# Performance work log

Measured on AMD Instinct MI355X. Metric: run time of the kernel, lower is better.

Reference implementation:

```python
import jax, jax.numpy as jnp
import numpy as np

B, S, FEAT, HID, H = 8, 1024, 1024, 1024, 8
DH = HID // H  # head dim = 128
MASK_VAL = -128.0  # mask_val = -2**7 (soft additive mask, per original code)


def setup_inputs() -> dict:
    key = jax.random.key(0)
    ks = jax.random.split(key, 4)
    scale = 0.02
    return {
        "queries": jax.random.normal(ks[0], (B, S, FEAT), dtype=jnp.float32),
        "Wq": jax.random.normal(ks[1], (FEAT, HID), dtype=jnp.float32) * scale,
        "bq": jnp.zeros((HID,), dtype=jnp.float32),
        "Wk": jax.random.normal(ks[2], (FEAT, HID), dtype=jnp.float32) * scale,
        "bk": jnp.zeros((HID,), dtype=jnp.float32),
        "Wv": jax.random.normal(ks[3], (FEAT, HID), dtype=jnp.float32) * scale,
        "bv": jnp.zeros((HID,), dtype=jnp.float32),
    }


def reference(queries, Wq, bq, Wk, bk, Wv, bv):
    # Self-attention: keys = values = queries (torch forward defaults)
    q = queries @ Wq + bq  # [B,S,HID]
    k = queries @ Wk + bk
    v = queries @ Wv + bv
    # split heads: chunk along last dim == reshape (B,S,H,DH)
    qh = q.reshape(B, S, H, DH)
    kh = k.reshape(B, S, H, DH)
    vh = v.reshape(B, S, H, DH)
    # exp-scaled-dot score (non-standard: exp BEFORE mask/softmax)
    logits = jnp.einsum("bqhd,bkhd->bhqk", qh, kh) / np.float32(np.sqrt(DH))
    score = jnp.exp(logits)
    # soft additive causal mask: upper triangle (diag=1) gets -128
    mask = jnp.triu(jnp.full((S, S), MASK_VAL, dtype=score.dtype), k=1)
    att = jax.nn.softmax(score + mask, axis=-1)  # [B,H,S,S]
    ctx = jnp.einsum("bhqk,bkhd->bqhd", att, vh)  # [B,S,H,DH]
    # reverse heads: concat along last dim
    return ctx.reshape(B, S, HID)
```

## Files before the change

kernel.cpp:

```cpp
#include <hip/hip_runtime.h>


typedef __bf16 bf16x8 __attribute__((ext_vector_type(8)));
typedef float floatx4 __attribute__((ext_vector_type(4)));
typedef unsigned short u16;
typedef unsigned int u32;

#define RSCALE 0.08838834764831845f

__device__ __forceinline__ u16 f2b(float f) {
  union { float f; unsigned u; } v; v.f = f;
  return (u16)((v.u + 0x7FFFu + ((v.u >> 16) & 1u)) >> 16);
}

__device__ __forceinline__ void gld_lds16(const void* g, void* l) {
  __builtin_amdgcn_global_load_lds(
      (const __attribute__((address_space(1))) unsigned*)g,
      (__attribute__((address_space(3))) unsigned*)l, 16, 0, 0);
}

#define MFMA16(a, b, c) __builtin_amdgcn_mfma_f32_16x16x32_bf16(a, b, c, 0, 0, 0)

__global__ __launch_bounds__(256) void prep_kernel(
    const float4* __restrict__ X, u16* __restrict__ Xb,
    const float* __restrict__ Wq, const float* __restrict__ Wk,
    const float* __restrict__ Wv, u16* __restrict__ Wtb) {
  if (blockIdx.x < 8192) {
    unsigned i = blockIdx.x * 256u + threadIdx.x;
    float4 v = X[i];
    ushort4 o;
    o.x = f2b(v.x); o.y = f2b(v.y); o.z = f2b(v.z); o.w = f2b(v.w);
    *reinterpret_cast<ushort4*>(Xb + 4u * i) = o;
  } else {
    const int bid = blockIdx.x - 8192;
    const int mat = bid >> 10;
    const int bx = bid & 31, by = (bid >> 5) & 31;
    const float* W = (mat == 0) ? Wq : (mat == 1) ? Wk : Wv;
    u16* Wt = Wtb + (size_t)mat * (1024u * 1024u);
    __shared__ u16 tile[32][33];
    const int x = threadIdx.x & 31, y = threadIdx.x >> 5;
    const int kt = bx * 32, nt = by * 32;
#pragma unroll
    for (int i = 0; i < 4; ++i)
      tile[y + 8 * i][x] = f2b(W[(size_t)(kt + y + 8 * i) * 1024 + nt + x]);
    __syncthreads();
#pragma unroll
    for (int i = 0; i < 4; ++i)
      Wt[(size_t)(nt + y + 8 * i) * 1024 + kt + x] = tile[x][y + 8 * i];
  }
}

__global__ __launch_bounds__(256, 4) void gemm_qkv_kernel(
    const u16* __restrict__ Xb, const u16* __restrict__ Wtb,
    const float* __restrict__ bq, const float* __restrict__ bk,
    const float* __restrict__ bv, u16* __restrict__ Qh, u16* __restrict__ Kh,
    u16* __restrict__ Vt) {
  const int mat = blockIdx.z;
  const u16* __restrict__ Wt = Wtb + (size_t)mat * (1024u * 1024u);
  const float* __restrict__ bias = (mat == 0) ? bq : (mat == 1) ? bk : bv;

  const int m0 = blockIdx.x * 128;
  const int n0 = blockIdx.y * 128;

  __shared__ u16 As[2][128 * 32];
  __shared__ u16 Bs[2][128 * 32];

  const int tid = threadIdx.x;
  const int wid = tid >> 6;
  const int lane = tid & 63;
  const int quad = lane >> 4;
  const int l16 = lane & 15;
  const int wm = (wid & 1) * 64;
  const int wn = (wid >> 1) * 64;

  const floatx4 z4 = {0.f, 0.f, 0.f, 0.f};
  floatx4 acc[4][4];
#pragma unroll
  for (int i = 0; i < 4; ++i)
#pragma unroll
    for (int j = 0; j < 4; ++j) acc[i][j] = z4;

  const int srow = lane >> 2;
  const int sg = (lane & 3) ^ ((lane >> 4) & 3);

  auto stage = [&](int b, int k0) {
#pragma unroll
    for (int c = 0; c < 2; ++c) {
      const int r0 = wid * 32 + c * 16;
      gld_lds16(Xb + (size_t)(m0 + r0 + srow) * 1024 + k0 + sg * 8,
                As[b] + r0 * 32);
      gld_lds16(Wt + (size_t)(n0 + r0 + srow) * 1024 + k0 + sg * 8,
                Bs[b] + r0 * 32);
    }
  };

  stage(0, 0);
  const int phys = (quad ^ ((l16 >> 2) & 3)) * 8;

  for (int i = 0; i < 32; ++i) {
    __syncthreads();
    if (i < 31) stage((i + 1) & 1, (i + 1) * 32);

    const u16* __restrict__ Ab = As[i & 1];
    const u16* __restrict__ Bb = Bs[i & 1];
    bf16x8 af[4], bfr[4];
#pragma unroll
    for (int ii = 0; ii < 4; ++ii)
      af[ii] = *(const bf16x8*)(Ab + (wm + ii * 16 + l16) * 32 + phys);
#pragma unroll
    for (int j = 0; j < 4; ++j)
      bfr[j] = *(const bf16x8*)(Bb + (wn + j * 16 + l16) * 32 + phys);
#pragma unroll
    for (int ii = 0; ii < 4; ++ii)
#pragma unroll
      for (int j = 0; j < 4; ++j)
        acc[ii][j] = MFMA16(af[ii], bfr[j], acc[ii][j]);
  }

  const int b = m0 >> 10;
  const int h = n0 >> 7;
  const int sbase = (m0 & 1023) + wm;
  float bv4[4];
#pragma unroll
  for (int j = 0; j < 4; ++j) bv4[j] = bias[n0 + wn + j * 16 + l16];

  if (mat < 2) {
    u16* outp = (mat == 0 ? Qh : Kh) + (size_t)(b * 8 + h) * 1024 * 128;
#pragma unroll
    for (int i = 0; i < 4; ++i)
#pragma unroll
      for (int j = 0; j < 4; ++j) {
        const int d = wn + j * 16 + l16;
#pragma unroll
        for (int r = 0; r < 4; ++r) {
          const int s = sbase + i * 16 + quad * 4 + r;
          outp[(size_t)s * 128 + d] = f2b(acc[i][j][r] + bv4[j]);
        }
      }
  } else {
    u16* outp = Vt + (size_t)(b * 8 + h) * 128 * 1024;
#pragma unroll
    for (int i = 0; i < 4; ++i)
#pragma unroll
      for (int j = 0; j < 4; ++j) {
        const int d = wn + j * 16 + l16;
        const int s = sbase + i * 16 + quad * 4;
        ushort4 pk;
        pk.x = f2b(acc[i][j][0] + bv4[j]);
        pk.y = f2b(acc[i][j][1] + bv4[j]);
        pk.z = f2b(acc[i][j][2] + bv4[j]);
        pk.w = f2b(acc[i][j][3] + bv4[j]);
        *(ushort4*)(outp + (size_t)d * 1024 + s) = pk;
      }
  }
}

__global__ __launch_bounds__(256, 4) void attn_kernel(const u16* __restrict__ Qh,
                                                      const u16* __restrict__ Kh,
                                                      const u16* __restrict__ Vt,
                                                      float* __restrict__ out) {
  const int id = blockIdx.x;
  const int bh = (id & 7) * 8 + ((id >> 3) & 7);
  const int qt = 15 - (id >> 6);
  const int q0 = qt * 64;

  const int tid = threadIdx.x;
  const int wid = tid >> 6;
  const int lane = tid & 63;
  const int quad = lane >> 4;
  const int l16 = lane & 15;

  __shared__ u16 Ks[2][32 * 128];
  __shared__ u16 Vs[2][128 * 32];
  __shared__ u16 Ps[4 * 16 * 32];

  const u16* __restrict__ Qbase = Qh + (size_t)bh * 1024 * 128;
  const u16* __restrict__ Kbase = Kh + (size_t)bh * 1024 * 128;
  const u16* __restrict__ Vbase = Vt + (size_t)bh * 128 * 1024;

  const int qw = q0 + wid * 16;
  const int qrow = qw + l16;

  bf16x8 qf[4];
#pragma unroll
  for (int c = 0; c < 4; ++c)
    qf[c] = *(const bf16x8*)(Qbase + (size_t)qrow * 128 + c * 32 + quad * 8);

  const floatx4 z4 = {0.f, 0.f, 0.f, 0.f};
  floatx4 o[8];
#pragma unroll
  for (int dt = 0; dt < 8; ++dt) o[dt] = z4;
  float lacc = 0.f;

  const int krow = lane >> 4;
  const int kg = l16;
  const int vrow = lane >> 2;
  const int vg = (lane & 3) ^ ((lane >> 4) & 3);

  auto stage = [&](int b, int k0) {
#pragma unroll
    for (int c = 0; c < 2; ++c) {
      const int r0 = wid * 8 + c * 4;
      const int row = r0 + krow;
      gld_lds16(Kbase + (size_t)(k0 + row) * 128 + ((kg ^ (row & 15)) * 8),
                Ks[b] + r0 * 128);
    }
#pragma unroll
    for (int c = 0; c < 2; ++c) {
      const int r0 = wid * 32 + c * 16;
      gld_lds16(Vbase + (size_t)(r0 + vrow) * 1024 + k0 + vg * 8,
                Vs[b] + r0 * 32);
    }
  };

  const int n = (q0 + 64) >> 5;
  stage(0, 0);

  const int s4 = (l16 >> 2) & 3;

  for (int i = 0; i < n; ++i) {
    const int k0 = i << 5;
    __syncthreads();
    if (i + 1 < n) stage((i + 1) & 1, k0 + 32);

    if (k0 <= qrow - l16 + 15) {
      const u16* __restrict__ Kb = Ks[i & 1];
      const u16* __restrict__ Vb = Vs[i & 1];

      floatx4 st[2];
#pragma unroll
      for (int f = 0; f < 2; ++f) {
        bf16x8 kf[4];
#pragma unroll
        for (int c = 0; c < 4; ++c)
          kf[c] = *(const bf16x8*)(Kb + (f * 16 + l16) * 128 +
                                   (((c * 4 + quad) ^ l16) * 8));
        st[f] = z4;
#pragma unroll
        for (int c = 0; c < 4; ++c) st[f] = MFMA16(kf[c], qf[c], st[f]);
      }

#pragma unroll
      for (int f = 0; f < 2; ++f) {
        const int kb = k0 + f * 16 + quad * 4;
        float p[4];
#pragma unroll
        for (int r = 0; r < 4; ++r) {
          const float e = fminf(__expf(st[f][r] * RSCALE), 85.f);
          p[r] = (kb + r > qrow) ? 0.f : __expf(e);
        }
        lacc += (p[0] + p[1]) + (p[2] + p[3]);
        uint2 pk;
        pk.x = (u32)f2b(p[0]) | ((u32)f2b(p[1]) << 16);
        pk.y = (u32)f2b(p[2]) | ((u32)f2b(p[3]) << 16);
        *(uint2*)((char*)Ps + wid * 1024 + l16 * 64 +
                  ((f * 2 + (quad >> 1)) ^ s4) * 16 + (quad & 1) * 8) = pk;
      }
      asm volatile("s_waitcnt lgkmcnt(0)" ::: "memory");

      const bf16x8 pa = *(const bf16x8*)((char*)Ps + wid * 1024 + l16 * 64 +
                                         (quad ^ s4) * 16);
#pragma unroll
      for (int dt = 0; dt < 8; ++dt) {
        const bf16x8 vf = *(const bf16x8*)(Vb + (dt * 16 + l16) * 32 +
                                           (quad ^ s4) * 8);
        o[dt] = MFMA16(vf, pa, o[dt]);
      }
    }
  }

  float s = lacc;
  s += __shfl_xor(s, 16);
  s += __shfl_xor(s, 32);
  const float linv = 1.0f / s;

  float* outp = out + (size_t)(bh >> 3) * 1024 * 1024 + (bh & 7) * 128;
#pragma unroll
  for (int dt = 0; dt < 8; ++dt) {
    float4 v;
    v.x = o[dt][0] * linv;
    v.y = o[dt][1] * linv;
    v.z = o[dt][2] * linv;
    v.w = o[dt][3] * linv;
    *(float4*)(outp + (size_t)qrow * 1024 + dt * 16 + quad * 4) = v;
  }
}

extern "C" void kernel_launch(void* const* d_in, const int* in_sizes, int n_in,
                              void* d_out, int out_size, void* d_ws,
                              size_t ws_size, hipStream_t stream) {
  const float* X = (const float*)d_in[0];
  const float* Wq = (const float*)d_in[1];
  const float* bq = (const float*)d_in[2];
  const float* Wk = (const float*)d_in[3];
  const float* bk = (const float*)d_in[4];
  const float* Wv = (const float*)d_in[5];
  const float* bv = (const float*)d_in[6];
  float* out = (float*)d_out;

  char* ws = (char*)d_ws;
  u16* Xb  = (u16*)(ws);
  u16* Wtb = (u16*)(ws + (16u << 20));
  u16* Qh  = (u16*)(ws + (22u << 20));
  u16* Kh  = (u16*)(ws + (38u << 20));
  u16* Vt  = (u16*)(ws + (54u << 20));

  prep_kernel<<<8192 + 3072, 256, 0, stream>>>((const float4*)X, Xb, Wq, Wk,
                                               Wv, Wtb);
  dim3 gg(64, 8, 3);
  gemm_qkv_kernel<<<gg, 256, 0, stream>>>(Xb, Wtb, bq, bk, bv, Qh, Kh, Vt);
  attn_kernel<<<1024, 256, 0, stream>>>(Qh, Kh, Vt, out);
}
```

Before: 202.2 us.

## Load B/V operands directly from global and widen K-step to 64

In the QKV GEMM, the weight tile is no longer staged through LDS; each wave loads its B fragments straight from global memory into registers, and the A tile's K-step is doubled to 64 with a new XOR swizzle. In attention, V is read directly from global per MFMA and only K is staged in LDS, now in 64-key tiles processed as two 32-key halves with an early break on the causal boundary. The aim is to cut LDS traffic and barriers per K step. The cost is uncoalesced, latency-exposed global loads in the inner loops that depend on cache hits.

Measured after the change: 292.0 us. +44.4%, slower.

```diff
diff --git a/kernel.cpp b/kernel.cpp
--- a/kernel.cpp
+++ b/kernel.cpp
@@ -62,8 +62,7 @@
   const int m0 = blockIdx.x * 128;
   const int n0 = blockIdx.y * 128;
 
-  __shared__ u16 As[2][128 * 32];
-  __shared__ u16 Bs[2][128 * 32];
+  __shared__ u16 As[2][128 * 64];
 
   const int tid = threadIdx.x;
   const int wid = tid >> 6;
@@ -80,41 +79,50 @@
 #pragma unroll
     for (int j = 0; j < 4; ++j) acc[i][j] = z4;
 
-  const int srow = lane >> 2;
-  const int sg = (lane & 3) ^ ((lane >> 4) & 3);
-
-  auto stage = [&](int b, int k0) {
-#pragma unroll
-    for (int c = 0; c < 2; ++c) {
-      const int r0 = wid * 32 + c * 16;
-      gld_lds16(Xb + (size_t)(m0 + r0 + srow) * 1024 + k0 + sg * 8,
-                As[b] + r0 * 32);
-      gld_lds16(Wt + (size_t)(n0 + r0 + srow) * 1024 + k0 + sg * 8,
-                Bs[b] + r0 * 32);
+  const int srow = wid * 32;
+  const int lrow = lane >> 3;
+  const int gblk = (lane & 7) ^ lrow;
+
+  auto stageA = [&](int b, int k0) {
+#pragma unroll
+    for (int c = 0; c < 4; ++c) {
+      const int row = srow + c * 8 + lrow;
+      gld_lds16(Xb + (size_t)(m0 + row) * 1024 + k0 + gblk * 8,
+                As[b] + (srow + c * 8) * 64);
     }
   };
 
-  stage(0, 0);
-  const int phys = (quad ^ ((l16 >> 2) & 3)) * 8;
-
-  for (int i = 0; i < 32; ++i) {
+  const u16* Brow[4];
+#pragma unroll
+  for (int j = 0; j < 4; ++j)
+    Brow[j] = Wt + (size_t)(n0 + wn + j * 16 + l16) * 1024 + quad * 8;
+
+  stageA(0, 0);
+
+  for (int i = 0; i < 16; ++i) {
     __syncthreads();
-    if (i < 31) stage((i + 1) & 1, (i + 1) * 32);
+    const int k0 = i * 64;
+    bf16x8 b0[4], b1[4];
+#pragma unroll
+    for (int j = 0; j < 4; ++j) b0[j] = *(const bf16x8*)(Brow[j] + k0);
+#pragma unroll
+    for (int j = 0; j < 4; ++j) b1[j] = *(const bf16x8*)(Brow[j] + k0 + 32);
+    if (i < 15) stageA((i + 1) & 1, k0 + 64);
 
     const u16* __restrict__ Ab = As[i & 1];
-    const u16* __restrict__ Bb = Bs[i & 1];
-    bf16x8 af[4], bfr[4];
-#pragma unroll
-    for (int ii = 0; ii < 4; ++ii)
-      af[ii] = *(const bf16x8*)(Ab + (wm + ii * 16 + l16) * 32 + phys);
-#pragma unroll
-    for (int j = 0; j < 4; ++j)
-      bfr[j] = *(const bf16x8*)(Bb + (wn + j * 16 + l16) * 32 + phys);
-#pragma unroll
-    for (int ii = 0; ii < 4; ++ii)
-#pragma unroll
-      for (int j = 0; j < 4; ++j)
-        acc[ii][j] = MFMA16(af[ii], bfr[j], acc[ii][j]);
+#pragma unroll
+    for (int c = 0; c < 2; ++c) {
+      const int phys = ((c * 4 + quad) ^ (l16 & 7)) * 8;
+      bf16x8 af[4];
+#pragma unroll
+      for (int ii = 0; ii < 4; ++ii)
+        af[ii] = *(const bf16x8*)(Ab + (wm + ii * 16 + l16) * 64 + phys);
+#pragma unroll
+      for (int ii = 0; ii < 4; ++ii)
+#pragma unroll
+        for (int j = 0; j < 4; ++j)
+          acc[ii][j] = MFMA16(af[ii], c ? b1[j] : b0[j], acc[ii][j]);
+    }
   }
 
   const int b = m0 >> 10;
@@ -170,9 +178,8 @@
   const int quad = lane >> 4;
   const int l16 = lane & 15;
 
-  __shared__ u16 Ks[2][32 * 128];
-  __shared__ u16 Vs[2][128 * 32];
-  __shared__ u16 Ps[4 * 16 * 32];
+  __shared__ u16 Ks[2][64 * 128];
+  __shared__ u16 Ps[4][16 * 32];
 
   const u16* __restrict__ Qbase = Qh + (size_t)bh * 1024 * 128;
   const u16* __restrict__ Kbase = Kh + (size_t)bh * 1024 * 128;
@@ -192,78 +199,65 @@
   for (int dt = 0; dt < 8; ++dt) o[dt] = z4;
   float lacc = 0.f;
 
-  const int krow = lane >> 4;
-  const int kg = l16;
-  const int vrow = lane >> 2;
-  const int vg = (lane & 3) ^ ((lane >> 4) & 3);
-
-  auto stage = [&](int b, int k0) {
-#pragma unroll
-    for (int c = 0; c < 2; ++c) {
-      const int r0 = wid * 8 + c * 4;
-      const int row = r0 + krow;
-      gld_lds16(Kbase + (size_t)(k0 + row) * 128 + ((kg ^ (row & 15)) * 8),
+  auto stageK = [&](int b, int k0) {
+#pragma unroll
+    for (int c = 0; c < 4; ++c) {
+      const int r0 = wid * 16 + c * 4;
+      const int row = r0 + quad;
+      gld_lds16(Kbase + (size_t)(k0 + row) * 128 + ((l16 ^ (c * 4 + quad)) * 8),
                 Ks[b] + r0 * 128);
     }
-#pragma unroll
-    for (int c = 0; c < 2; ++c) {
-      const int r0 = wid * 32 + c * 16;
-      gld_lds16(Vbase + (size_t)(r0 + vrow) * 1024 + k0 + vg * 8,
-                Vs[b] + r0 * 32);
-    }
   };
 
-  const int n = (q0 + 64) >> 5;
-  stage(0, 0);
-
-  const int s4 = (l16 >> 2) & 3;
+  const int n = qt + 1;
+  stageK(0, 0);
+  const int s4 = l16 & 3;
 
   for (int i = 0; i < n; ++i) {
-    const int k0 = i << 5;
+    const int k0 = i << 6;
     __syncthreads();
-    if (i + 1 < n) stage((i + 1) & 1, k0 + 32);
-
-    if (k0 <= qrow - l16 + 15) {
-      const u16* __restrict__ Kb = Ks[i & 1];
-      const u16* __restrict__ Vb = Vs[i & 1];
-
-      floatx4 st[2];
-#pragma unroll
-      for (int f = 0; f < 2; ++f) {
+    if (i + 1 < n) stageK((i + 1) & 1, k0 + 64);
+
+    const u16* __restrict__ Kb = Ks[i & 1];
+
+#pragma unroll
+    for (int half = 0; half < 2; ++half) {
+      if (k0 + half * 32 > qw + 15) break;
+
+#pragma unroll
+      for (int f2 = 0; f2 < 2; ++f2) {
+        const int f = half * 2 + f2;
         bf16x8 kf[4];
 #pragma unroll
         for (int c = 0; c < 4; ++c)
           kf[c] = *(const bf16x8*)(Kb + (f * 16 + l16) * 128 +
                                    (((c * 4 + quad) ^ l16) * 8));
-        st[f] = z4;
-#pragma unroll
-        for (int c = 0; c < 4; ++c) st[f] = MFMA16(kf[c], qf[c], st[f]);
-      }
-
-#pragma unroll
-      for (int f = 0; f < 2; ++f) {
+        floatx4 st = z4;
+#pragma unroll
+        for (int c = 0; c < 4; ++c) st = MFMA16(kf[c], qf[c], st);
         const int kb = k0 + f * 16 + quad * 4;
         float p[4];
 #pragma unroll
         for (int r = 0; r < 4; ++r) {
-          const float e = fminf(__expf(st[f][r] * RSCALE), 85.f);
+          const float e = fminf(__expf(st[r] * RSCALE), 85.f);
           p[r] = (kb + r > qrow) ? 0.f : __expf(e);
         }
         lacc += (p[0] + p[1]) + (p[2] + p[3]);
         uint2 pk;
         pk.x = (u32)f2b(p[0]) | ((u32)f2b(p[1]) << 16);
         pk.y = (u32)f2b(p[2]) | ((u32)f2b(p[3]) << 16);
-        *(uint2*)((char*)Ps + wid * 1024 + l16 * 64 +
-                  ((f * 2 + (quad >> 1)) ^ s4) * 16 + (quad & 1) * 8) = pk;
+        *(uint2*)((char*)Ps[wid] + l16 * 64 +
+                  (((f2 * 2 + (quad >> 1)) ^ s4) * 16) + (quad & 1) * 8) = pk;
       }
       asm volatile("s_waitcnt lgkmcnt(0)" ::: "memory");
 
-      const bf16x8 pa = *(const bf16x8*)((char*)Ps + wid * 1024 + l16 * 64 +
-                                         (quad ^ s4) * 16);
+      const bf16x8 pa = *(const bf16x8*)((char*)Ps[wid] + l16 * 64 +
+                                         ((quad ^ s4) * 16));
+      const size_t voff = (size_t)k0 + half * 32 + quad * 8;
 #pragma unroll
       for (int dt = 0; dt < 8; ++dt) {
-        const bf16x8 vf = *(const bf16x8*)(Vb + (dt * 16 + l16) * 32 +
-                                           (quad ^ s4) * 8);
+        const bf16x8 vf =
+            *(const bf16x8*)(Vbase + (size_t)(dt * 16 + l16) * 1024 + voff);
         o[dt] = MFMA16(vf, pa, o[dt]);
       }
     }
```
